# Kernel tuning notes

Measured on AMD Instinct MI355X. Metric: run time of the kernel, lower is better.

## Reference

```python
import jax, jax.numpy as jnp
import numpy as np

N_NODES = 50000
N_PAIRS = 200000
HID1 = 256
HID2 = 32


def gcn_conv(x, src, dst, W, b, n):
    # PyG GCNConv: project, add self-loops, sym-normalize, scatter-add to dst.
    sl = jnp.arange(n, dtype=src.dtype)
    s = jnp.concatenate([src, sl])
    d = jnp.concatenate([dst, sl])
    deg = jnp.zeros((n,), x.dtype).at[d].add(1.0)
    dinv = jax.lax.rsqrt(deg)  # deg >= 1 due to self-loops
    xw = x @ W  # [n, out]
    msg = xw[s] * (dinv[s] * dinv[d])[:, None]  # [E+n, out]
    out = jax.ops.segment_sum(msg, d, num_segments=n)
    return out + b


def setup_inputs() -> dict:
    key = jax.random.key(0)
    ks = jax.random.split(key, 16)
    inp = {
        "x": jax.random.randint(ks[0], (N_NODES,), 0, N_NODES),
        "edge1": jax.random.randint(ks[1], (2, 1600000), 0, N_NODES),
        "pos": jax.random.randint(ks[2], (N_PAIRS, 2), 0, N_NODES),
        "idx": jax.random.randint(ks[3], (N_PAIRS,), 0, N_PAIRS),
        "ei2": jax.random.randint(ks[4], (2, 1600000), 0, N_PAIRS),
        "emb_table": jax.random.normal(ks[5], (N_NODES + 1, HID1), jnp.float32) * 0.02,
        "W1": jax.random.normal(ks[6], (HID1, HID2), jnp.float32) * (1.0 / np.sqrt(HID1)),
        "b1": jnp.zeros((HID2,), jnp.float32),
        "W2a": jax.random.normal(ks[7], (HID2, HID2), jnp.float32) * (1.0 / np.sqrt(HID2)),
        "b2a": jnp.zeros((HID2,), jnp.float32),
        "W2b": jax.random.normal(ks[8], (HID2, HID2), jnp.float32) * (1.0 / np.sqrt(HID2)),
        "b2b": jnp.zeros((HID2,), jnp.float32),
        "Wp": jax.random.normal(ks[9], (HID2, 1), jnp.float32) * (1.0 / np.sqrt(HID2)),
        "bp": jnp.zeros((1,), jnp.float32),
    }
    return inp


def reference(x, edge1, pos, idx, ei2, emb_table, W1, b1, W2a, b2a, W2b, b2b, Wp, bp):
    # eval mode: all Dropouts are identity; no LayerNorm/GraphNorm (default flags False)
    h = emb_table[x]  # [N, HID1] embedding lookup (squeeze is no-op for 1D ids)
    # conv1s: single GCNConv HID1 -> HID2 + ReLU
    h = jax.nn.relu(gcn_conv(h, edge1[0], edge1[1], W1, b1, N_NODES))
    # pairwise gather-multiply over pos
    h = h[pos[:, 0]] * h[pos[:, 1]]  # [M, HID2]
    # conv2s / conv2s_r on the pair graph (edge2 = ei2, edge2_r = flipped)
    h = (jax.nn.relu(gcn_conv(h, ei2[0], ei2[1], W2a, b2a, N_PAIRS))
         + jax.nn.relu(gcn_conv(h, ei2[1], ei2[0], W2b, b2b, N_PAIRS)))
    # gather by idx, then multiply consecutive (even, odd) rows
    h = h[idx]  # [2Q, HID2]
    h = h[0::2] * h[1::2]  # [Q, HID2]
    return h @ Wp + bp  # [Q, 1]
```

## Files before the change

kernel.cpp:

```cpp
#include <hip/hip_runtime.h>
#include <hip/hip_fp16.h>
#include <math.h>


#define SL     256
#define SLOG   8
#define SL1    64
#define SLOG1  6
#define CAP    2432
#define SHIFT  18
#define NMASK  ((1 << SHIFT) - 1)
#define BCH    8192
#define BT     1024
#define EPT    8
#define MAXSL2 1024
#define PB     64
#define EROW   264
#define G2B    2048
#define G2T    256
#define G2I    4

typedef short bf16x8 __attribute__((ext_vector_type(8)));
typedef float f32x4 __attribute__((ext_vector_type(4)));

static __device__ __forceinline__ unsigned short f2bf(float f) {
    union { float f; unsigned u; } v;
    v.f = f;
    unsigned r = v.u + 0x7FFF + ((v.u >> 16) & 1);
    return (unsigned short)(r >> 16);
}
static __device__ __forceinline__ float bf2f(unsigned short h) {
    return __uint_as_float(((unsigned)h) << 16);
}
static __device__ __forceinline__ float bflo(unsigned u) { return __uint_as_float(u << 16); }
static __device__ __forceinline__ float bfhi(unsigned u) { return __uint_as_float(u & 0xFFFF0000u); }

static __device__ __forceinline__ float4 bfacc(float4 a, uint2 w) {
    a.x += bflo(w.x);
    a.y += bfhi(w.x);
    a.z += bflo(w.y);
    a.w += bfhi(w.y);
    return a;
}
static __device__ __forceinline__ float4 hacc(float4 a, uint2 w) {
    float2 f0 = __half22float2(*(__half2*)&w.x);
    float2 f1 = __half22float2(*(__half2*)&w.y);
    a.x += f0.x;
    a.y += f0.y;
    a.z += f1.x;
    a.w += f1.y;
    return a;
}
static __device__ __forceinline__ float4 h2f4(uint2 w) {
    float2 f0 = __half22float2(*(__half2*)&w.x);
    float2 f1 = __half22float2(*(__half2*)&w.y);
    float4 r = {f0.x, f0.y, f1.x, f1.y};
    return r;
}
static __device__ __forceinline__ uint2 f42h(float4 f) {
    __half2 h0 = __floats2half2_rn(f.x, f.y);
    __half2 h1 = __floats2half2_rn(f.z, f.w);
    uint2 r = {*(unsigned*)&h0, *(unsigned*)&h1};
    return r;
}

__global__ __launch_bounds__(256) void k_init(int* __restrict__ bumpF,
                                              int* __restrict__ bumpR,
                                              int* __restrict__ bump1,
                                              int NS2, int NS1) {
    int i = blockIdx.x * 256 + threadIdx.x;
    if (i < NS2) {
        bumpF[i] = i * CAP;
        bumpR[i] = i * CAP;
    }
    if (i < NS1) bump1[i] = i * CAP;
}

__global__ __launch_bounds__(BT) void k_build(const int* __restrict__ s2,
                                              const int* __restrict__ d2,
                                              const int* __restrict__ s1,
                                              const int* __restrict__ d1,
                                              int* bumpF, int* bumpR, int* bump1,
                                              int* __restrict__ bktF,
                                              int* __restrict__ bktR,
                                              int* __restrict__ bkt1,
                                              const float* __restrict__ W1,
                                              const float* __restrict__ W2a,
                                              const float* __restrict__ W2b,
                                              unsigned short* __restrict__ Wbhi,
                                              unsigned short* __restrict__ Wblo,
                                              unsigned short* __restrict__ W2ah,
                                              unsigned short* __restrict__ W2al,
                                              unsigned short* __restrict__ W2bh,
                                              unsigned short* __restrict__ W2bl,
                                              int E2, int E1, int NS2, int NS1,
                                              int NB2, int NB1) {
    __shared__ int stag[BCH];
    __shared__ unsigned short stag2[BCH];
    __shared__ int lbF[MAXSL2];
    __shared__ int lbR[MAXSL2];
    __shared__ int bgF[MAXSL2], bgR[MAXSL2];
    __shared__ int wsum[BT / 64];
    int tid = threadIdx.x, bid = blockIdx.x;
    int lane = tid & 63, wid = tid >> 6;

    auto exscan = [&](int v) -> int {
        int sc = v;
#pragma unroll
        for (int d = 1; d < 64; d <<= 1) {
            int t = __shfl_up(sc, d, 64);
            if (lane >= d) sc += t;
        }
        if (lane == 63) wsum[wid] = sc;
        __syncthreads();
        int woff = 0;
        for (int w2 = 0; w2 < wid; w2++) woff += wsum[w2];
        __syncthreads();
        return woff + sc - v;
    };

    if (bid < NB2) {
        if (tid < NS2) { lbF[tid] = 0; lbR[tid] = 0; }
        __syncthreads();
        int eb = bid * BCH;
        int n = E2 - eb; if (n > BCH) n = BCH;
        int sv[EPT], dv[EPT], ofF[EPT], ofR[EPT];
#pragma unroll
        for (int k = 0; k < EPT; k++) {
            int i = k * BT + tid;
            if (i < n) {
                sv[k] = s2[eb + i];
                dv[k] = d2[eb + i];
                ofF[k] = atomicAdd(&lbF[dv[k] >> SLOG], 1);
                ofR[k] = atomicAdd(&lbR[sv[k] >> SLOG], 1);
            }
        }
        __syncthreads();
        int cF = (tid < NS2) ? lbF[tid] : 0;
        int cR = (tid < NS2) ? lbR[tid] : 0;
        int preF = exscan(cF);
        int preR = exscan(cR);
        if (tid < NS2) {
            lbF[tid] = preF;
            lbR[tid] = preR;
            bgF[tid] = cF ? atomicAdd(&bumpF[tid], cF) : 0;
            bgR[tid] = cR ? atomicAdd(&bumpR[tid], cR) : 0;
        }
        __syncthreads();
#pragma unroll
        for (int k = 0; k < EPT; k++) {
            int i = k * BT + tid;
            if (i < n) {
                int sf = dv[k] >> SLOG;
                int p = lbF[sf] + ofF[k];
                stag[p] = ((dv[k] & (SL - 1)) << SHIFT) | sv[k];
                stag2[p] = (unsigned short)sf;
            }
        }
        __syncthreads();
        for (int i = tid; i < n; i += BT) {
            int sf = stag2[i];
            int gp = bgF[sf] + (i - lbF[sf]);
            if (gp < (sf + 1) * CAP) bktF[gp] = stag[i];
        }
        __syncthreads();
#pragma unroll
        for (int k = 0; k < EPT; k++) {
            int i = k * BT + tid;
            if (i < n) {
                int sr = sv[k] >> SLOG;
                int p = lbR[sr] + ofR[k];
                stag[p] = ((sv[k] & (SL - 1)) << SHIFT) | dv[k];
                stag2[p] = (unsigned short)sr;
            }
        }
        __syncthreads();
        for (int i = tid; i < n; i += BT) {
            int sr = stag2[i];
            int gp = bgR[sr] + (i - lbR[sr]);
            if (gp < (sr + 1) * CAP) bktR[gp] = stag[i];
        }
    } else if (bid < NB2 + NB1) {
        if (tid < NS1) lbF[tid] = 0;
        __syncthreads();
        int eb = (bid - NB2) * BCH;
        int n = E1 - eb; if (n > BCH) n = BCH;
        int sv[EPT], dv[EPT], of[EPT];
#pragma unroll
        for (int k = 0; k < EPT; k++) {
            int i = k * BT + tid;
            if (i < n) {
                sv[k] = s1[eb + i];
                dv[k] = d1[eb + i];
                of[k] = atomicAdd(&lbF[dv[k] >> SLOG1], 1);
            }
        }
        __syncthreads();
        int c = (tid < NS1) ? lbF[tid] : 0;
        int pre = exscan(c);
        if (tid < NS1) {
            lbF[tid] = pre;
            bgF[tid] = c ? atomicAdd(&bump1[tid], c) : 0;
        }
        __syncthreads();
#pragma unroll
        for (int k = 0; k < EPT; k++) {
            int i = k * BT + tid;
            if (i < n) {
                int sf = dv[k] >> SLOG1;
                int p = lbF[sf] + of[k];
                stag[p] = ((dv[k] & (SL1 - 1)) << SHIFT) | sv[k];
                stag2[p] = (unsigned short)sf;
            }
        }
        __syncthreads();
        for (int i = tid; i < n; i += BT) {
            int sf = stag2[i];
            int gp = bgF[sf] + (i - lbF[sf]);
            if (gp < (sf + 1) * CAP) bkt1[gp] = stag[i];
        }
    } else {
        int i = (bid - NB2 - NB1) * BT + tid;
        if (i < 8192) {
            int k = i >> 5, c = i & 31;
            float w = W1[i];
            unsigned short hi = f2bf(w);
            unsigned short lo = f2bf(w - bf2f(hi));
            Wbhi[c * 256 + k] = hi;
            Wblo[c * 256 + k] = lo;
        }
        if (i < 1024) {
            int k = i >> 5, c = i & 31;
            float wa = W2a[i], wb = W2b[i];
            unsigned short ha = f2bf(wa);
            unsigned short hb = f2bf(wb);
            W2ah[c * 32 + k] = ha;
            W2al[c * 32 + k] = f2bf(wa - bf2f(ha));
            W2bh[c * 32 + k] = hb;
            W2bl[c * 32 + k] = f2bf(wb - bf2f(hb));
        }
    }
}

__global__ __launch_bounds__(256) void k_sort(int* __restrict__ bkt1, const int* __restrict__ bump1,
                                              float* __restrict__ dinv1, int* __restrict__ beg1,
                                              int* __restrict__ cnt1,
                                              int* __restrict__ bktF, const int* __restrict__ bumpF,
                                              float* __restrict__ dinvF, int* __restrict__ begF,
                                              int* __restrict__ cntF,
                                              int* __restrict__ bktR, const int* __restrict__ bumpR,
                                              float* __restrict__ dinvR, int* __restrict__ begR,
                                              int* __restrict__ cntR,
                                              int NS1, int NS2, int N1, int NP) {
    __shared__ int A[CAP];
    __shared__ int S[CAP];
    __shared__ int hN[SL], hD[SL];
    __shared__ int wsum[4];
    int bid = blockIdx.x, tid = threadIdx.x;
    int s, sls, N;
    int* bkt;
    const int* bump;
    float* dinv;
    int* beg;
    int* cntA;
    if (bid < NS1) {
        s = bid;
        bkt = bkt1; bump = bump1; dinv = dinv1; beg = beg1; cntA = cnt1;
        sls = SL1; N = N1;
    } else if (bid < NS1 + NS2) {
        s = bid - NS1;
        bkt = bktF; bump = bumpF; dinv = dinvF; beg = begF; cntA = cntF;
        sls = SL; N = NP;
    } else {
        s = bid - NS1 - NS2;
        bkt = bktR; bump = bumpR; dinv = dinvR; beg = begR; cntA = cntR;
        sls = SL; N = NP;
    }
    hN[tid] = 0;
    hD[tid] = 0;
    __syncthreads();
    int cnt = bump[s] - s * CAP;
    if (cnt > CAP) cnt = CAP;
    int* b = bkt + (size_t)s * CAP;
    for (int i = tid; i < cnt; i += 256) {
        int e = b[i];
        atomicAdd(&hN[(e & NMASK) >> 10], 1);
        atomicAdd(&hD[e >> SHIFT], 1);
    }
    __syncthreads();
    int cn = hN[tid];
    int cd = hD[tid];
    int lane = tid & 63, wid = tid >> 6;
    auto exscan = [&](int v) -> int {
        int sc = v;
#pragma unroll
        for (int d = 1; d < 64; d <<= 1) {
            int t = __shfl_up(sc, d, 64);
            if (lane >= d) sc += t;
        }
        if (lane == 63) wsum[wid] = sc;
        __syncthreads();
        int woff = 0;
        for (int w = 0; w < wid; w++) woff += wsum[w];
        __syncthreads();
        return woff + sc - v;
    };
    int preN = exscan(cn);
    int preD = exscan(cd);
    hN[tid] = preN;
    hD[tid] = preD;
    if (tid < sls) {
        int v = s * sls + tid;
        if (v < N) {
            dinv[v] = 1.f / sqrtf((float)cd + 1.f);
            beg[v] = s * CAP + preD;
            cntA[v] = cd;
        }
    }
    __syncthreads();
    for (int i = tid; i < cnt; i += 256) {
        int e = b[i];
        int p = atomicAdd(&hN[(e & NMASK) >> 10], 1);
        A[p] = e;
    }
    __syncthreads();
    for (int i = tid; i < cnt; i += 256) {
        int e = A[i];
        int p = atomicAdd(&hD[e >> SHIFT], 1);
        S[p] = e & NMASK;
    }
    __syncthreads();
    for (int i = tid; i < cnt; i += 256) b[i] = S[i];
}

__global__ __launch_bounds__(256) void k_xw1(const int* __restrict__ x,
                                             const float* __restrict__ emb,
                                             const unsigned short* __restrict__ Wbhi,
                                             const unsigned short* __restrict__ Wblo,
                                             const float* __restrict__ dinv1,
                                             __half* __restrict__ y1, int N) {
    __shared__ unsigned short sEhi[32 * EROW];
    __shared__ unsigned short sElo[32 * EROW];
    int tid = threadIdx.x;
    int lane = tid & 63, wv = tid >> 6;
    int r0 = blockIdx.x * 32;
    const float4* emb4 = (const float4*)emb;
#pragma unroll
    for (int p = 0; p < 8; p++) {
        int row = p * 4 + wv;
        int r = r0 + row;
        int xr = x[(r < N) ? r : 0];
        float4 e = emb4[(size_t)xr * 64 + lane];
        unsigned short h0 = f2bf(e.x), h1 = f2bf(e.y), h2 = f2bf(e.z), h3 = f2bf(e.w);
        ushort4 hi = {h0, h1, h2, h3};
        ushort4 lo = {f2bf(e.x - bf2f(h0)), f2bf(e.y - bf2f(h1)),
                      f2bf(e.z - bf2f(h2)), f2bf(e.w - bf2f(h3))};
        *(ushort4*)&sEhi[row * EROW + lane * 4] = hi;
        *(ushort4*)&sElo[row * EROW + lane * 4] = lo;
    }
    __syncthreads();
    int col = lane & 15, quad = lane >> 4;
    int rowtile = wv >> 1, ntile = wv & 1;
    f32x4 acc = {0.f, 0.f, 0.f, 0.f};
    const unsigned short* arow_hi = &sEhi[(rowtile * 16 + col) * EROW + quad * 8];
    const unsigned short* arow_lo = &sElo[(rowtile * 16 + col) * EROW + quad * 8];
    const unsigned short* bh = Wbhi + (ntile * 16 + col) * 256 + quad * 8;
    const unsigned short* bl = Wblo + (ntile * 16 + col) * 256 + quad * 8;
#pragma unroll
    for (int kb = 0; kb < 256; kb += 32) {
        bf16x8 ahi = *(const bf16x8*)(arow_hi + kb);
        bf16x8 alo = *(const bf16x8*)(arow_lo + kb);
        bf16x8 bhv = *(const bf16x8*)(bh + kb);
        bf16x8 blv = *(const bf16x8*)(bl + kb);
        acc = __builtin_amdgcn_mfma_f32_16x16x32_bf16(ahi, bhv, acc, 0, 0, 0);
        acc = __builtin_amdgcn_mfma_f32_16x16x32_bf16(alo, bhv, acc, 0, 0, 0);
        acc = __builtin_amdgcn_mfma_f32_16x16x32_bf16(ahi, blv, acc, 0, 0, 0);
    }
#pragma unroll
    for (int reg = 0; reg < 4; reg++) {
        int grow = r0 + rowtile * 16 + quad * 4 + reg;
        if (grow < N) {
            float dv = dinv1[grow];
            y1[grow * 32 + ntile * 16 + col] = __float2half(acc[reg] * dv);
        }
    }
}

static __device__ __forceinline__ float4 gcn_sum_h8(const int* __restrict__ adj, int bg, int end,
                                                    const uint2* __restrict__ y2, int q,
                                                    float4 acc) {
    float4 a1 = {0.f, 0.f, 0.f, 0.f};
    int i = bg;
    for (; i + 8 <= end; i += 8) {
        int u0 = adj[i], u1 = adj[i + 1], u2 = adj[i + 2], u3 = adj[i + 3];
        int u4 = adj[i + 4], u5 = adj[i + 5], u6 = adj[i + 6], u7 = adj[i + 7];
        uint2 w0 = y2[u0 * 8 + q];
        uint2 w1 = y2[u1 * 8 + q];
        uint2 w2 = y2[u2 * 8 + q];
        uint2 w3 = y2[u3 * 8 + q];
        uint2 w4 = y2[u4 * 8 + q];
        uint2 w5 = y2[u5 * 8 + q];
        uint2 w6 = y2[u6 * 8 + q];
        uint2 w7 = y2[u7 * 8 + q];
        acc = hacc(acc, w0);
        a1 = hacc(a1, w1);
        acc = hacc(acc, w2);
        a1 = hacc(a1, w3);
        acc = hacc(acc, w4);
        a1 = hacc(a1, w5);
        acc = hacc(acc, w6);
        a1 = hacc(a1, w7);
    }
    for (; i + 4 <= end; i += 4) {
        int u0 = adj[i], u1 = adj[i + 1], u2 = adj[i + 2], u3 = adj[i + 3];
        uint2 w0 = y2[u0 * 8 + q];
        uint2 w1 = y2[u1 * 8 + q];
        uint2 w2 = y2[u2 * 8 + q];
        uint2 w3 = y2[u3 * 8 + q];
        acc = hacc(acc, w0);
        a1 = hacc(a1, w1);
        acc = hacc(acc, w2);
        a1 = hacc(a1, w3);
    }
    for (; i < end; i++) acc = hacc(acc, y2[adj[i] * 8 + q]);
    acc.x += a1.x;
    acc.y += a1.y;
    acc.z += a1.z;
    acc.w += a1.w;
    return acc;
}

static __device__ __forceinline__ float4 gcn_sum_bf(const int* __restrict__ adj, int bg, int end,
                                                    const uint2* __restrict__ y2, int q,
                                                    float4 acc) {
    float4 a1 = {0.f, 0.f, 0.f, 0.f};
    int i = bg;
    for (; i + 4 <= end; i += 4) {
        int u0 = adj[i], u1 = adj[i + 1], u2 = adj[i + 2], u3 = adj[i + 3];
        uint2 w0 = y2[u0 * 8 + q];
        uint2 w1 = y2[u1 * 8 + q];
        uint2 w2 = y2[u2 * 8 + q];
        uint2 w3 = y2[u3 * 8 + q];
        acc = bfacc(acc, w0);
        a1 = bfacc(a1, w1);
        acc = bfacc(acc, w2);
        a1 = bfacc(a1, w3);
    }
    for (; i < end; i++) acc = bfacc(acc, y2[adj[i] * 8 + q]);
    acc.x += a1.x;
    acc.y += a1.y;
    acc.z += a1.z;
    acc.w += a1.w;
    return acc;
}

__global__ __launch_bounds__(256) void k_gath1(const int* __restrict__ adj,
                                               const int* __restrict__ beg,
                                               const int* __restrict__ cntA,
                                               const float* __restrict__ dinv,
                                               const __half* __restrict__ y1,
                                               __half* __restrict__ out1, int N) {
    int gid = blockIdx.x * 256 + threadIdx.x;
    int v = gid >> 3, q = gid & 7;
    if (v >= N) return;
    int bg = beg[v];
    int end = bg + cntA[v];
    float dv = dinv[v];
    const uint2* y2 = (const uint2*)y1;
    float4 acc = {0.f, 0.f, 0.f, 0.f};
    acc = hacc(acc, y2[v * 8 + q]);
    acc = gcn_sum_h8(adj, bg, end, y2, q, acc);
    acc.x *= dv;
    acc.y *= dv;
    acc.z *= dv;
    acc.w *= dv;
    ((uint2*)out1)[v * 8 + q] = f42h(acc);
}

__global__ __launch_bounds__(G2T, 8) void k_gath2p(const int* __restrict__ adjF,
                                                   const int* __restrict__ begF,
                                                   const int* __restrict__ cntF,
                                                   const float* __restrict__ dinvF,
                                                   const unsigned short* __restrict__ ya,
                                                   const int* __restrict__ adjR,
                                                   const int* __restrict__ begR,
                                                   const int* __restrict__ cntR,
                                                   const float* __restrict__ dinvR,
                                                   const unsigned short* __restrict__ yb,
                                                   const float* __restrict__ b2a,
                                                   const float* __restrict__ b2b,
                                                   __half* __restrict__ h3, int NP) {
    int tid0 = blockIdx.x * G2T + threadIdx.x;
    const int stride = G2B * G2T;
    const uint2* ya2 = (const uint2*)ya;
    const uint2* yb2 = (const uint2*)yb;
    float4 hF[G2I];
#pragma unroll
    for (int k = 0; k < G2I; k++) {
        int gid = tid0 + k * stride;
        int v = gid >> 3, q = gid & 7;
        float4 acc = {0.f, 0.f, 0.f, 0.f};
        if (v < NP) {
            acc = bfacc(acc, ya2[v * 8 + q]);
            int bF = begF[v];
            acc = gcn_sum_bf(adjF, bF, bF + cntF[v], ya2, q, acc);
            float dvF = dinvF[v];
            float4 ba = ((const float4*)b2a)[q];
            acc.x = fmaxf(fmaf(acc.x, dvF, ba.x), 0.f);
            acc.y = fmaxf(fmaf(acc.y, dvF, ba.y), 0.f);
            acc.z = fmaxf(fmaf(acc.z, dvF, ba.z), 0.f);
            acc.w = fmaxf(fmaf(acc.w, dvF, ba.w), 0.f);
        }
        hF[k] = acc;
    }
#pragma unroll
    for (int k = 0; k < G2I; k++) {
        int gid = tid0 + k * stride;
        int v = gid >> 3, q = gid & 7;
        if (v < NP) {
            float4 aR = {0.f, 0.f, 0.f, 0.f};
            aR = bfacc(aR, yb2[v * 8 + q]);
            int bR = begR[v];
            aR = gcn_sum_bf(adjR, bR, bR + cntR[v], yb2, q, aR);
            float dvR = dinvR[v];
            float4 bb = ((const float4*)b2b)[q];
            float4 h;
            h.x = hF[k].x + fmaxf(fmaf(aR.x, dvR, bb.x), 0.f);
            h.y = hF[k].y + fmaxf(fmaf(aR.y, dvR, bb.y), 0.f);
            h.z = hF[k].z + fmaxf(fmaf(aR.z, dvR, bb.z), 0.f);
            h.w = hF[k].w + fmaxf(fmaf(aR.w, dvR, bb.w), 0.f);
            ((uint2*)h3)[v * 8 + q] = f42h(h);
        }
    }
}

__global__ __launch_bounds__(256) void k_xw2(const int* __restrict__ pos,
                                             const __half* __restrict__ out1,
                                             const float* __restrict__ b1,
                                             const unsigned short* __restrict__ W2ah,
                                             const unsigned short* __restrict__ W2al,
                                             const unsigned short* __restrict__ W2bh,
                                             const unsigned short* __restrict__ W2bl,
                                             const float* __restrict__ dinvF,
                                             const float* __restrict__ dinvR,
                                             unsigned short* __restrict__ ya,
                                             unsigned short* __restrict__ yb,
                                             int NP) {
    __shared__ unsigned short sHhi[PB * 32];
    __shared__ unsigned short sHlo[PB * 32];
    __shared__ int sPos[PB * 2];
    int tid = threadIdx.x;
    int p0 = blockIdx.x * PB;
    if (tid < PB * 2) {
        int gi = p0 * 2 + tid;
        sPos[tid] = (gi < NP * 2) ? pos[gi] : 0;
    }
    __syncthreads();
    const uint2* o12 = (const uint2*)out1;
    int q = tid & 7;
    float4 bq = ((const float4*)b1)[q];
#pragma unroll
    for (int half = 0; half < 2; half++) {
        int p = half * 32 + (tid >> 3);
        int ra = sPos[2 * p] * 8, rb = sPos[2 * p + 1] * 8;
        float4 ea = h2f4(o12[ra + q]);
        float4 eb = h2f4(o12[rb + q]);
        float4 h;
        h.x = fmaxf(ea.x + bq.x, 0.f) * fmaxf(eb.x + bq.x, 0.f);
        h.y = fmaxf(ea.y + bq.y, 0.f) * fmaxf(eb.y + bq.y, 0.f);
        h.z = fmaxf(ea.z + bq.z, 0.f) * fmaxf(eb.z + bq.z, 0.f);
        h.w = fmaxf(ea.w + bq.w, 0.f) * fmaxf(eb.w + bq.w, 0.f);
        unsigned short h0 = f2bf(h.x), h1 = f2bf(h.y), h2 = f2bf(h.z), h3 = f2bf(h.w);
        ushort4 hi = {h0, h1, h2, h3};
        ushort4 lo = {f2bf(h.x - bf2f(h0)), f2bf(h.y - bf2f(h1)),
                      f2bf(h.z - bf2f(h2)), f2bf(h.w - bf2f(h3))};
        *(ushort4*)&sHhi[p * 32 + q * 4] = hi;
        *(ushort4*)&sHlo[p * 32 + q * 4] = lo;
    }
    __syncthreads();
    int lane = tid & 63, wv = tid >> 6;
    int col = lane & 15, quad = lane >> 4;
    bf16x8 ahi = *(const bf16x8*)&sHhi[(wv * 16 + col) * 32 + quad * 8];
    bf16x8 alo = *(const bf16x8*)&sHlo[(wv * 16 + col) * 32 + quad * 8];
    f32x4 accA[2], accB[2];
#pragma unroll
    for (int nt = 0; nt < 2; nt++) {
        int off = (nt * 16 + col) * 32 + quad * 8;
        bf16x8 bah = *(const bf16x8*)(W2ah + off);
        bf16x8 bal = *(const bf16x8*)(W2al + off);
        bf16x8 bbh = *(const bf16x8*)(W2bh + off);
        bf16x8 bbl = *(const bf16x8*)(W2bl + off);
        f32x4 z = {0.f, 0.f, 0.f, 0.f};
        f32x4 a = __builtin_amdgcn_mfma_f32_16x16x32_bf16(ahi, bah, z, 0, 0, 0);
        a = __builtin_amdgcn_mfma_f32_16x16x32_bf16(alo, bah, a, 0, 0, 0);
        a = __builtin_amdgcn_mfma_f32_16x16x32_bf16(ahi, bal, a, 0, 0, 0);
        accA[nt] = a;
        f32x4 b = __builtin_amdgcn_mfma_f32_16x16x32_bf16(ahi, bbh, z, 0, 0, 0);
        b = __builtin_amdgcn_mfma_f32_16x16x32_bf16(alo, bbh, b, 0, 0, 0);
        b = __builtin_amdgcn_mfma_f32_16x16x32_bf16(ahi, bbl, b, 0, 0, 0);
        accB[nt] = b;
    }
#pragma unroll
    for (int reg = 0; reg < 4; reg++) {
        int p = wv * 16 + quad * 4 + reg;
        int pg = p0 + p;
        if (pg < NP) {
            float dA = dinvF[pg], dB = dinvR[pg];
#pragma unroll
            for (int nt = 0; nt < 2; nt++) {
                ya[pg * 32 + nt * 16 + col] = f2bf(accA[nt][reg] * dA);
                yb[pg * 32 + nt * 16 + col] = f2bf(accB[nt][reg] * dB);
            }
        }
    }
}

__global__ __launch_bounds__(256) void k_final(const int* __restrict__ idx,
                                               const __half* __restrict__ h3,
                                               const float* __restrict__ Wp,
                                               const float* __restrict__ bp,
                                               float* __restrict__ out, int Q) {
    int gid = blockIdx.x * 256 + threadIdx.x;
    int qi = gid >> 3, q = gid & 7;
    if (qi >= Q) return;
    int i0 = idx[2 * qi] * 8, i1 = idx[2 * qi + 1] * 8;
    float4 wp = ((const float4*)Wp)[q];
    const uint2* H = (const uint2*)h3;
    float4 h0 = h2f4(H[i0 + q]), h1 = h2f4(H[i1 + q]);
    float s = h0.x * h1.x * wp.x + h0.y * h1.y * wp.y + h0.z * h1.z * wp.z + h0.w * h1.w * wp.w;
    s += __shfl_xor(s, 1);
    s += __shfl_xor(s, 2);
    s += __shfl_xor(s, 4);
    if (q == 0) out[qi] = s + bp[0];
}

extern "C" void kernel_launch(void* const* d_in, const int* in_sizes, int n_in,
                              void* d_out, int out_size, void* d_ws, size_t ws_size,
                              hipStream_t stream) {
    const int* x    = (const int*)d_in[0];
    const int* e1   = (const int*)d_in[1];
    const int* pos  = (const int*)d_in[2];
    const int* idx  = (const int*)d_in[3];
    const int* e2   = (const int*)d_in[4];
    const float* emb = (const float*)d_in[5];
    const float* W1  = (const float*)d_in[6];
    const float* b1  = (const float*)d_in[7];
    const float* W2a = (const float*)d_in[8];
    const float* b2a = (const float*)d_in[9];
    const float* W2b = (const float*)d_in[10];
    const float* b2b = (const float*)d_in[11];
    const float* Wp  = (const float*)d_in[12];
    const float* bp  = (const float*)d_in[13];

    const int N1 = in_sizes[0];
    const int E1 = in_sizes[1] / 2;
    const int NP = in_sizes[3];
    const int E2 = in_sizes[4] / 2;
    const int Q  = out_size;
    (void)n_in; (void)ws_size;

    const int NS1 = (N1 + SL1 - 1) >> SLOG1;
    const int NS2 = (NP + SL - 1) >> SLOG;

    char* w = (char*)d_ws;
    size_t o = 0;
    auto alloc = [&](size_t bytes) { size_t r = o; o += (bytes + 255) & ~(size_t)255; return r; };
    float* dinv1  = (float*)(w + alloc((size_t)(N1 + 2 * NP) * 4));
    float* dinv2f = dinv1 + N1;
    float* dinv2r = dinv2f + NP;
    int* beg1  = (int*)(w + alloc((size_t)(N1 + 2 * NP) * 4));
    int* beg2f = beg1 + N1;
    int* beg2r = beg2f + NP;
    int* cnt1  = (int*)(w + alloc((size_t)(N1 + 2 * NP) * 4));
    int* cnt2f = cnt1 + N1;
    int* cnt2r = cnt2f + NP;
    int* bumpF = (int*)(w + alloc((size_t)(2 * NS2 + NS1) * 4));
    int* bumpR = bumpF + NS2;
    int* bump1 = bumpR + NS2;
    unsigned short* Wbhi = (unsigned short*)(w + alloc(8192 * 2));
    unsigned short* Wblo = (unsigned short*)(w + alloc(8192 * 2));
    unsigned short* W2ah = (unsigned short*)(w + alloc(1024 * 2));
    unsigned short* W2al = (unsigned short*)(w + alloc(1024 * 2));
    unsigned short* W2bh = (unsigned short*)(w + alloc(1024 * 2));
    unsigned short* W2bl = (unsigned short*)(w + alloc(1024 * 2));
    int* bktF = (int*)(w + alloc((size_t)NS2 * CAP * 4));
    int* bktR = (int*)(w + alloc((size_t)NS2 * CAP * 4));
    int* bkt1 = (int*)(w + alloc((size_t)NS1 * CAP * 4));
    __half* out1 = (__half*)(w + alloc((size_t)N1 * 32 * 2));
    __half* y1   = (__half*)(w + alloc((size_t)N1 * 32 * 2));
    unsigned short* ya = (unsigned short*)(w + alloc((size_t)NP * 32 * 2));
    unsigned short* yb = (unsigned short*)(w + alloc((size_t)NP * 32 * 2));
    __half* h3  = (__half*)(w + alloc((size_t)NP * 32 * 2));

    const int B = 256;
    auto cdiv = [](long long a, long long b) { return (int)((a + b - 1) / b); };
    const int NB2 = cdiv(E2, BCH), NB1 = cdiv(E1, BCH);
    const int NBW = cdiv(8192, BT);

    k_init<<<cdiv(NS2 > NS1 ? NS2 : NS1, B), B, 0, stream>>>(bumpF, bumpR, bump1, NS2, NS1);
    k_build<<<NB2 + NB1 + NBW, BT, 0, stream>>>(e2, e2 + E2, e1, e1 + E1,
                                                bumpF, bumpR, bump1, bktF, bktR, bkt1,
                                                W1, W2a, W2b, Wbhi, Wblo,
                                                W2ah, W2al, W2bh, W2bl,
                                                E2, E1, NS2, NS1, NB2, NB1);
    k_sort<<<NS1 + 2 * NS2, B, 0, stream>>>(bkt1, bump1, dinv1, beg1, cnt1,
                                            bktF, bumpF, dinv2f, beg2f, cnt2f,
                                            bktR, bumpR, dinv2r, beg2r, cnt2r,
                                            NS1, NS2, N1, NP);
    k_xw1<<<cdiv(N1, 32), B, 0, stream>>>(x, emb, Wbhi, Wblo, dinv1, y1, N1);
    k_gath1<<<cdiv((long long)N1 * 8, B), B, 0, stream>>>(bkt1, beg1, cnt1, dinv1, y1, out1, N1);
    k_xw2<<<cdiv(NP, PB), B, 0, stream>>>(pos, out1, b1, W2ah, W2al, W2bh, W2bl,
                                          dinv2f, dinv2r, ya, yb, NP);
    k_gath2p<<<G2B, G2T, 0, stream>>>(bktF, beg2f, cnt2f, dinv2f, ya,
                                      bktR, beg2r, cnt2r, dinv2r, yb,
                                      b2a, b2b, h3, NP);
    k_final<<<cdiv((long long)Q * 8, B), B, 0, stream>>>(idx, h3, Wp, bp, (float*)d_out, Q);
}
```

Measured before the change: 279.0 us.

## Replace two-pass bucket radix sort with single counting pass; memset bump counters

The per-bucket sort in k_sort drops the first pass that ordered edges by source high bits and keeps only one counting-sort pass by local destination. That removes one histogram, one scan and one shared-memory scatter per bucket. The cost is that neighbours within a destination segment are no longer grouped by source, which may reduce gather locality in the later kernels. The k_init kernel is replaced by a hipMemsetAsync that zeroes the bump counters, with the per-bucket base offset now added in k_build. That memset assumes bumpF, bumpR and bump1 are laid out contiguously in the workspace.

After: 280.7 us. Within noise of the previous version (+0.6%).

```diff
diff --git a/kernel.cpp b/kernel.cpp
--- a/kernel.cpp
+++ b/kernel.cpp
@@ -62,18 +62,6 @@
     __half2 h1 = __floats2half2_rn(f.z, f.w);
     uint2 r = {*(unsigned*)&h0, *(unsigned*)&h1};
     return r;
-}
-
-__global__ __launch_bounds__(256) void k_init(int* __restrict__ bumpF,
-                                              int* __restrict__ bumpR,
-                                              int* __restrict__ bump1,
-                                              int NS2, int NS1) {
-    int i = blockIdx.x * 256 + threadIdx.x;
-    if (i < NS2) {
-        bumpF[i] = i * CAP;
-        bumpR[i] = i * CAP;
-    }
-    if (i < NS1) bump1[i] = i * CAP;
 }
 
 __global__ __launch_bounds__(BT) void k_build(const int* __restrict__ s2,
@@ -143,8 +131,8 @@
         if (tid < NS2) {
             lbF[tid] = preF;
             lbR[tid] = preR;
-            bgF[tid] = cF ? atomicAdd(&bumpF[tid], cF) : 0;
-            bgR[tid] = cR ? atomicAdd(&bumpR[tid], cR) : 0;
+            bgF[tid] = (cF ? atomicAdd(&bumpF[tid], cF) : 0) + tid * CAP;
+            bgR[tid] = (cR ? atomicAdd(&bumpR[tid], cR) : 0) + tid * CAP;
         }
         __syncthreads();
 #pragma unroll
@@ -200,7 +188,7 @@
         int pre = exscan(c);
         if (tid < NS1) {
             lbF[tid] = pre;
-            bgF[tid] = c ? atomicAdd(&bump1[tid], c) : 0;
+            bgF[tid] = (c ? atomicAdd(&bump1[tid], c) : 0) + tid * CAP;
         }
         __syncthreads();
 #pragma unroll
@@ -252,9 +240,8 @@
                                               float* __restrict__ dinvR, int* __restrict__ begR,
                                               int* __restrict__ cntR,
                                               int NS1, int NS2, int N1, int NP) {
-    __shared__ int A[CAP];
-    __shared__ int S[CAP];
-    __shared__ int hN[SL], hD[SL];
+    __shared__ int sorted[CAP];
+    __shared__ int hist[SL], cursor[SL];
     __shared__ int wsum[4];
     int bid = blockIdx.x, tid = threadIdx.x;
     int s, sls, N;
@@ -276,61 +263,44 @@
         bkt = bktR; bump = bumpR; dinv = dinvR; beg = begR; cntA = cntR;
         sls = SL; N = NP;
     }
-    hN[tid] = 0;
-    hD[tid] = 0;
-    __syncthreads();
-    int cnt = bump[s] - s * CAP;
+    hist[tid] = 0;
+    __syncthreads();
+    int cnt = bump[s];
     if (cnt > CAP) cnt = CAP;
     int* b = bkt + (size_t)s * CAP;
-    for (int i = tid; i < cnt; i += 256) {
-        int e = b[i];
-        atomicAdd(&hN[(e & NMASK) >> 10], 1);
-        atomicAdd(&hD[e >> SHIFT], 1);
-    }
-    __syncthreads();
-    int cn = hN[tid];
-    int cd = hD[tid];
+    for (int i = tid; i < cnt; i += 256) atomicAdd(&hist[b[i] >> SHIFT], 1);
+    __syncthreads();
+    int c = (tid < sls) ? hist[tid] : 0;
+    int sc = c;
     int lane = tid & 63, wid = tid >> 6;
-    auto exscan = [&](int v) -> int {
-        int sc = v;
-#pragma unroll
-        for (int d = 1; d < 64; d <<= 1) {
-            int t = __shfl_up(sc, d, 64);
-            if (lane >= d) sc += t;
-        }
-        if (lane == 63) wsum[wid] = sc;
-        __syncthreads();
-        int woff = 0;
-        for (int w = 0; w < wid; w++) woff += wsum[w];
-        __syncthreads();
-        return woff + sc - v;
-    };
-    int preN = exscan(cn);
-    int preD = exscan(cd);
-    hN[tid] = preN;
-    hD[tid] = preD;
+#pragma unroll
+    for (int d = 1; d < 64; d <<= 1) {
+        int t = __shfl_up(sc, d, 64);
+        if (lane >= d) sc += t;
+    }
+    if (lane == 63) wsum[wid] = sc;
+    __syncthreads();
+    int woff = 0;
+    for (int w = 0; w < wid; w++) woff += wsum[w];
+    int pre = woff + sc - c;
+    cursor[tid] = pre;
     if (tid < sls) {
         int v = s * sls + tid;
         if (v < N) {
-            dinv[v] = 1.f / sqrtf((float)cd + 1.f);
-            beg[v] = s * CAP + preD;
-            cntA[v] = cd;
+            dinv[v] = 1.f / sqrtf((float)c + 1.f);
+            beg[v] = s * CAP + pre;
+            cntA[v] = c;
         }
     }
     __syncthreads();
     for (int i = tid; i < cnt; i += 256) {
-        int e = b[i];
-        int p = atomicAdd(&hN[(e & NMASK) >> 10], 1);
-        A[p] = e;
-    }
-    __syncthreads();
-    for (int i = tid; i < cnt; i += 256) {
-        int e = A[i];
-        int p = atomicAdd(&hD[e >> SHIFT], 1);
-        S[p] = e & NMASK;
-    }
-    __syncthreads();
-    for (int i = tid; i < cnt; i += 256) b[i] = S[i];
+        int pair = b[i];
+        int dl = pair >> SHIFT;
+        int p = atomicAdd(&cursor[dl], 1);
+        sorted[p] = pair & NMASK;
+    }
+    __syncthreads();
+    for (int i = tid; i < cnt; i += 256) b[i] = sorted[i];
 }
 
 __global__ __launch_bounds__(256) void k_xw1(const int* __restrict__ x,
@@ -697,7 +667,7 @@
     const int NB2 = cdiv(E2, BCH), NB1 = cdiv(E1, BCH);
     const int NBW = cdiv(8192, BT);
 
-    k_init<<<cdiv(NS2 > NS1 ? NS2 : NS1, B), B, 0, stream>>>(bumpF, bumpR, bump1, NS2, NS1);
+    hipMemsetAsync(bumpF, 0, (size_t)(2 * NS2 + NS1) * 4, stream);
     k_build<<<NB2 + NB1 + NBW, BT, 0, stream>>>(e2, e2 + E2, e1, e1 + E1,
                                                 bumpF, bumpR, bump1, bktF, bktR, bkt1,
                                                 W1, W2a, W2b, Wbhi, Wblo,
```
